# Kernel tuning notes

Measured on AMD Instinct MI355X. Metric: run time of the kernel, lower is better.

Reference implementation:

```python
import jax, jax.numpy as jnp
import numpy as np

B = 256      # complexes per batch
MOL_N = 40   # atoms per ligand
PRO_N = 400  # residues per protein pocket
HID = 64     # hid_dim
HEADS = 8


def setup_inputs() -> dict:
    key = jax.random.key(0)
    ks = jax.random.split(key, 8)
    M, P = B * MOL_N, B * PRO_N
    # create_index(mol_size, pro_size) with uniform sizes: all-pairs per complex
    mol_index = np.repeat(np.arange(M, dtype=np.int64), PRO_N)
    pro_ids = np.arange(P, dtype=np.int64).reshape(B, PRO_N)
    pro_index = np.broadcast_to(pro_ids[:, None, :], (B, MOL_N, PRO_N)).reshape(-1)
    mol_batch = np.repeat(np.arange(B, dtype=np.int64), MOL_N)
    return {
        "mol_feats": jax.random.normal(ks[0], (M, HID), jnp.float32),
        "pro_feats": jax.random.normal(ks[1], (P, HID), jnp.float32),
        "spatial_feats": jax.random.normal(ks[2], (P, HID), jnp.float32),
        "sigma_w": jax.random.normal(ks[3], (2 * HID, HEADS), jnp.float32) * 0.08,
        "sigma_b": jnp.zeros((HEADS,), jnp.float32),
        "mu_w": jax.random.normal(ks[4], (2 * HID, HEADS), jnp.float32) * 0.08,
        "mu_b": jnp.zeros((HEADS,), jnp.float32),
        "w1": jax.random.normal(ks[5], (HEADS, 2 * HEADS), jnp.float32) * 0.3,
        "b1": jnp.zeros((2 * HEADS,), jnp.float32),
        "w2": jax.random.normal(ks[6], (2 * HEADS, 1), jnp.float32) * 0.25,
        "b2": jnp.zeros((1,), jnp.float32),
        "mol_index": jnp.asarray(mol_index),
        "pro_index": jnp.asarray(pro_index),
        "mol_batch": jnp.asarray(mol_batch),
        "num_graphs": B,
    }


def reference(mol_feats, pro_feats, spatial_feats, sigma_w, sigma_b, mu_w, mu_b,
              w1, b1, w2, b2, mol_index, pro_index, mol_batch, num_graphs):
    hid = mol_feats.shape[1]
    pro = pro_feats * spatial_feats  # pro_feats * spatial_feats
    # Linear on concat([mol[i], pro[j]]) == per-side projections summed after gather.
    # Avoids materializing the [E, 2*hid] concat; same math as nn.Linear(2*hid, heads).
    mol_s = mol_feats @ sigma_w[:hid]   # [M, heads]
    pro_s = pro @ sigma_w[hid:]         # [P, heads]
    mol_m = mol_feats @ mu_w[:hid]
    pro_m = pro @ mu_w[hid:]
    sigma = jax.nn.elu(mol_s[mol_index] + pro_s[pro_index] + sigma_b) + 1.1  # [E, heads]
    mu = jax.nn.elu(mol_m[mol_index] + pro_m[pro_index] + mu_b) + 1.0       # [E, heads]
    # scatter_sum over pairs -> mol atoms, then mol atoms -> graphs
    y = jax.ops.segment_sum(mu, mol_index, num_segments=mol_feats.shape[0])  # [M, heads]
    y = jax.ops.segment_sum(y, mol_batch, num_segments=num_graphs) * 0.001   # [B, heads]
    y = jax.nn.elu(y @ w1 + b1)
    y_pred = y @ w2 + b2  # [B, 1]
    return mu, sigma, y_pred
```

## Files before the change

### kernel.cpp

```cpp
#include <hip/hip_runtime.h>

#define HID    64
#define HEADS  8
#define MOL_N  40
#define PRO_N  400
#define NGRAPH 256

__device__ __forceinline__ float elu_plus(float x, float c) {
    return x > 0.0f ? x + c : __expf(x) - 1.0f + c;
}

__global__ __launch_bounds__(256) void proj_kernel(
    const float* __restrict__ mol_feats, const float* __restrict__ pro_feats,
    const float* __restrict__ spatial,   const float* __restrict__ sigma_w,
    const float* __restrict__ sigma_b,   const float* __restrict__ mu_w,
    const float* __restrict__ mu_b,
    float* __restrict__ mol_s, float* __restrict__ mol_m,
    float* __restrict__ pro_s, float* __restrict__ pro_m,
    float* __restrict__ y_acc, int mol_blocks)
{
    __shared__ float rows[32][HID + 1];
    __shared__ float wsig[HID][HEADS];
    __shared__ float wmu [HID][HEADS];

    const int tid = threadIdx.x;
    const bool is_mol = (int)blockIdx.x < mol_blocks;

    if (blockIdx.x == 0) {
        for (int i = tid; i < NGRAPH * HEADS; i += 256) y_acc[i] = 0.0f;
    }

    const int wofs = is_mol ? 0 : HID * HEADS;
    for (int i = tid; i < HID * HEADS; i += 256) {
        wsig[i / HEADS][i % HEADS] = sigma_w[wofs + i];
        wmu [i / HEADS][i % HEADS] = mu_w  [wofs + i];
    }

    const int r0 = (is_mol ? (int)blockIdx.x : ((int)blockIdx.x - mol_blocks)) * 32;
    if (is_mol) {
        const float4* src = (const float4*)mol_feats + (size_t)r0 * (HID / 4);
        for (int i = tid; i < 32 * (HID / 4); i += 256) {
            float4 v = src[i];
            int lr = i / (HID / 4), k4 = (i % (HID / 4)) * 4;
            rows[lr][k4 + 0] = v.x; rows[lr][k4 + 1] = v.y;
            rows[lr][k4 + 2] = v.z; rows[lr][k4 + 3] = v.w;
        }
    } else {
        const float4* srcp = (const float4*)pro_feats + (size_t)r0 * (HID / 4);
        const float4* srcs = (const float4*)spatial   + (size_t)r0 * (HID / 4);
        for (int i = tid; i < 32 * (HID / 4); i += 256) {
            float4 a = srcp[i];
            float4 b = srcs[i];
            int lr = i / (HID / 4), k4 = (i % (HID / 4)) * 4;
            rows[lr][k4 + 0] = a.x * b.x; rows[lr][k4 + 1] = a.y * b.y;
            rows[lr][k4 + 2] = a.z * b.z; rows[lr][k4 + 3] = a.w * b.w;
        }
    }
    __syncthreads();

    const int lr = tid >> 3;
    const int h  = tid & 7;
    float as = 0.0f, am = 0.0f;
#pragma unroll
    for (int k = 0; k < HID; ++k) {
        float x = rows[lr][k];
        as += x * wsig[k][h];
        am += x * wmu [k][h];
    }
    const int gr = r0 + lr;
    if (is_mol) {
        mol_s[gr * HEADS + h] = as + sigma_b[h];
        mol_m[gr * HEADS + h] = am + mu_b[h];
    } else {
        pro_s[gr * HEADS + h] = as;
        pro_m[gr * HEADS + h] = am;
    }
}

__global__ __launch_bounds__(256) void edge_kernel(
    const float* __restrict__ mol_s, const float* __restrict__ mol_m,
    const float* __restrict__ pro_s, const float* __restrict__ pro_m,
    float* __restrict__ mu_out, float* __restrict__ sg_out,
    float* __restrict__ y_acc)
{
    const int m   = blockIdx.x;
    const int b   = m / MOL_N;
    const int tid = threadIdx.x;

    __shared__ float s_mol[16];
    __shared__ float s_hsum[HEADS];
    if (tid < 8)       s_mol[tid] = mol_s[m * HEADS + tid];
    else if (tid < 16) s_mol[tid] = mol_m[m * HEADS + (tid - 8)];
    if (tid < HEADS)   s_hsum[tid] = 0.0f;
    __syncthreads();

    const int q = tid & 1;
    float ms[4], mm[4];
#pragma unroll
    for (int k = 0; k < 4; ++k) {
        ms[k] = s_mol[q * 4 + k];
        mm[k] = s_mol[8 + q * 4 + k];
    }

    const float4* pm4 = (const float4*)pro_m + (size_t)b * PRO_N * 2;
    const float4* ps4 = (const float4*)pro_s + (size_t)b * PRO_N * 2;
    float4* mu4 = (float4*)mu_out + (size_t)m * PRO_N * 2;
    float4* sg4 = (float4*)sg_out + (size_t)m * PRO_N * 2;

    float acc[4] = {0.f, 0.f, 0.f, 0.f};
    for (int t = tid; t < PRO_N * 2; t += 256) {
        float4 p = pm4[t];
        float4 v;
        v.x = elu_plus(p.x + mm[0], 1.0f);
        v.y = elu_plus(p.y + mm[1], 1.0f);
        v.z = elu_plus(p.z + mm[2], 1.0f);
        v.w = elu_plus(p.w + mm[3], 1.0f);
        mu4[t] = v;
        acc[0] += v.x; acc[1] += v.y; acc[2] += v.z; acc[3] += v.w;
    }
    for (int t = tid; t < PRO_N * 2; t += 256) {
        float4 p = ps4[t];
        float4 v;
        v.x = elu_plus(p.x + ms[0], 1.1f);
        v.y = elu_plus(p.y + ms[1], 1.1f);
        v.z = elu_plus(p.z + ms[2], 1.1f);
        v.w = elu_plus(p.w + ms[3], 1.1f);
        sg4[t] = v;
    }

#pragma unroll
    for (int mask = 2; mask < 64; mask <<= 1) {
#pragma unroll
        for (int k = 0; k < 4; ++k) acc[k] += __shfl_xor(acc[k], mask, 64);
    }
    if ((tid & 63) < 2) {
#pragma unroll
        for (int k = 0; k < 4; ++k) atomicAdd(&s_hsum[q * 4 + k], acc[k]);
    }
    __syncthreads();
    if (tid < HEADS) atomicAdd(&y_acc[b * HEADS + tid], s_hsum[tid]);
}

__global__ __launch_bounds__(256) void head_kernel(
    const float* __restrict__ y_acc, const float* __restrict__ w1,
    const float* __restrict__ b1,    const float* __restrict__ w2,
    const float* __restrict__ b2,    float* __restrict__ y_pred)
{
    const int g = threadIdx.x;
    float y[HEADS];
#pragma unroll
    for (int h = 0; h < HEADS; ++h) y[h] = y_acc[g * HEADS + h] * 0.001f;
    float out = b2[0];
#pragma unroll
    for (int o = 0; o < 2 * HEADS; ++o) {
        float a = b1[o];
#pragma unroll
        for (int h = 0; h < HEADS; ++h) a += y[h] * w1[h * (2 * HEADS) + o];
        a = a > 0.0f ? a : __expf(a) - 1.0f;
        out += a * w2[o];
    }
    y_pred[g] = out;
}

extern "C" void kernel_launch(void* const* d_in, const int* in_sizes, int n_in,
                              void* d_out, int out_size, void* d_ws, size_t ws_size,
                              hipStream_t stream) {
    const float* mol_feats = (const float*)d_in[0];
    const float* pro_feats = (const float*)d_in[1];
    const float* spatial   = (const float*)d_in[2];
    const float* sigma_w   = (const float*)d_in[3];
    const float* sigma_b   = (const float*)d_in[4];
    const float* mu_w      = (const float*)d_in[5];
    const float* mu_b      = (const float*)d_in[6];
    const float* w1        = (const float*)d_in[7];
    const float* b1        = (const float*)d_in[8];
    const float* w2        = (const float*)d_in[9];
    const float* b2        = (const float*)d_in[10];

    const int M = in_sizes[0] / HID;
    const int P = in_sizes[1] / HID;
    const int E = in_sizes[11];

    float* ws    = (float*)d_ws;
    float* mol_s = ws;
    float* mol_m = mol_s + (size_t)M * HEADS;
    float* pro_s = mol_m + (size_t)M * HEADS;
    float* pro_m = pro_s + (size_t)P * HEADS;
    float* y_acc = pro_m + (size_t)P * HEADS;

    float* mu_out = (float*)d_out;
    float* sg_out = mu_out + (size_t)E * HEADS;
    float* y_pred = sg_out + (size_t)E * HEADS;

    const int mol_blocks = M / 32;
    const int pro_blocks = P / 32;

    proj_kernel<<<mol_blocks + pro_blocks, 256, 0, stream>>>(
        mol_feats, pro_feats, spatial, sigma_w, sigma_b, mu_w, mu_b,
        mol_s, mol_m, pro_s, pro_m, y_acc, mol_blocks);

    edge_kernel<<<M, 256, 0, stream>>>(
        mol_s, mol_m, pro_s, pro_m, mu_out, sg_out, y_acc);

    head_kernel<<<1, 256, 0, stream>>>(y_acc, w1, b1, w2, b2, y_pred);
}
```

Baseline: 355.2 us.

## Interleave graph block order, fuse mu/sigma loops, use nontemporal stores

Remaps block indices so consecutive blocks belong to different graphs, spreading the per-graph atomics and protein-row reads differently across the machine. Fuses the mu and sigma loops into one pass so both protein projections load together, and writes the large mu/sigma outputs with nontemporal stores so the write-only stream does not pollute the cache. The block remap may reduce L2 reuse of each graph's protein rows, since blocks sharing a graph are now 256 apart.

```diff
diff --git a/kernel.cpp b/kernel.cpp
--- a/kernel.cpp
+++ b/kernel.cpp
@@ -5,6 +5,8 @@
 #define MOL_N  40
 #define PRO_N  400
 #define NGRAPH 256
+
+typedef float vfloat4 __attribute__((ext_vector_type(4)));
 
 __device__ __forceinline__ float elu_plus(float x, float c) {
     return x > 0.0f ? x + c : __expf(x) - 1.0f + c;
@@ -83,8 +85,10 @@
     float* __restrict__ mu_out, float* __restrict__ sg_out,
     float* __restrict__ y_acc)
 {
-    const int m   = blockIdx.x;
-    const int b   = m / MOL_N;
+    const int bi  = blockIdx.x;
+    const int b   = bi & (NGRAPH - 1);
+    const int r   = bi >> 8;
+    const int m   = b * MOL_N + r;
     const int tid = threadIdx.x;
 
     __shared__ float s_mol[16];
@@ -102,30 +106,27 @@
         mm[k] = s_mol[8 + q * 4 + k];
     }
 
-    const float4* pm4 = (const float4*)pro_m + (size_t)b * PRO_N * 2;
-    const float4* ps4 = (const float4*)pro_s + (size_t)b * PRO_N * 2;
-    float4* mu4 = (float4*)mu_out + (size_t)m * PRO_N * 2;
-    float4* sg4 = (float4*)sg_out + (size_t)m * PRO_N * 2;
+    const vfloat4* pm4 = (const vfloat4*)pro_m + (size_t)b * PRO_N * 2;
+    const vfloat4* ps4 = (const vfloat4*)pro_s + (size_t)b * PRO_N * 2;
+    vfloat4* mu4 = (vfloat4*)mu_out + (size_t)m * PRO_N * 2;
+    vfloat4* sg4 = (vfloat4*)sg_out + (size_t)m * PRO_N * 2;
 
     float acc[4] = {0.f, 0.f, 0.f, 0.f};
     for (int t = tid; t < PRO_N * 2; t += 256) {
-        float4 p = pm4[t];
-        float4 v;
-        v.x = elu_plus(p.x + mm[0], 1.0f);
-        v.y = elu_plus(p.y + mm[1], 1.0f);
-        v.z = elu_plus(p.z + mm[2], 1.0f);
-        v.w = elu_plus(p.w + mm[3], 1.0f);
-        mu4[t] = v;
-        acc[0] += v.x; acc[1] += v.y; acc[2] += v.z; acc[3] += v.w;
-    }
-    for (int t = tid; t < PRO_N * 2; t += 256) {
-        float4 p = ps4[t];
-        float4 v;
-        v.x = elu_plus(p.x + ms[0], 1.1f);
-        v.y = elu_plus(p.y + ms[1], 1.1f);
-        v.z = elu_plus(p.z + ms[2], 1.1f);
-        v.w = elu_plus(p.w + ms[3], 1.1f);
-        sg4[t] = v;
+        vfloat4 pmv = pm4[t];
+        vfloat4 psv = ps4[t];
+        vfloat4 vmu, vsg;
+        vmu.x = elu_plus(pmv.x + mm[0], 1.0f);
+        vmu.y = elu_plus(pmv.y + mm[1], 1.0f);
+        vmu.z = elu_plus(pmv.z + mm[2], 1.0f);
+        vmu.w = elu_plus(pmv.w + mm[3], 1.0f);
+        vsg.x = elu_plus(psv.x + ms[0], 1.1f);
+        vsg.y = elu_plus(psv.y + ms[1], 1.1f);
+        vsg.z = elu_plus(psv.z + ms[2], 1.1f);
+        vsg.w = elu_plus(psv.w + ms[3], 1.1f);
+        __builtin_nontemporal_store(vmu, &mu4[t]);
+        __builtin_nontemporal_store(vsg, &sg4[t]);
+        acc[0] += vmu.x; acc[1] += vmu.y; acc[2] += vmu.z; acc[3] += vmu.w;
     }
 
 #pragma unroll
```

New measurement: 353.9 us. No clear change (-0.4%).
